# Optimization experiments

Measured on AMD Instinct MI355X. Metric: run time of the kernel, lower is better.

## Reference

```python
import jax, jax.numpy as jnp
import numpy as np

TABLE_SIZE = 524288
NUM_LEVELS = 16
MIN_RES = 16
MAX_RES = 2048
FEAT = 2
N_POINTS = 1048576

# Spatial-hash primes, wrapped to int32 exactly as the original module ends up doing
PRIMES = jnp.asarray(np.array([1, 2654435761, 805459861], dtype=np.uint32).astype(np.int32))

# Per-level grid resolutions (computed in float64 numpy at trace time, stored f32)
_levels_np = np.arange(NUM_LEVELS)
_growth = np.exp((np.log(MAX_RES) - np.log(MIN_RES)) / (NUM_LEVELS - 1))
SCALINGS = jnp.asarray(np.floor(MIN_RES * _growth ** _levels_np), dtype=jnp.float32)  # (L,)
HASH_OFFSET = jnp.arange(NUM_LEVELS, dtype=jnp.int32) * TABLE_SIZE  # (L,)

# Ceil(1)/floor(0) selector per corner, matching vertex_0..vertex_7 in the original
SEL = jnp.asarray(np.array([
    [1, 1, 1], [1, 1, 0], [1, 0, 1], [0, 1, 1],
    [1, 0, 0], [0, 1, 0], [0, 0, 1], [0, 0, 0]], dtype=bool))  # (8,3)


def setup_inputs() -> dict:
    key = jax.random.key(0)
    k1, k2 = jax.random.split(key)
    x = jax.random.uniform(k1, (N_POINTS, 3), dtype=jnp.float32)  # points in [0,1)^3
    hash_table = jax.random.normal(k2, (FEAT, TABLE_SIZE * NUM_LEVELS), dtype=jnp.float32)
    return {"x": x, "hash_table": hash_table}


def reference(x, hash_table):
    N = x.shape[0]
    scaled = x[:, None, :] * SCALINGS[None, :, None]          # (N, L, 3)
    c = jnp.ceil(scaled).astype(jnp.int32)                    # (N, L, 3)
    f = jnp.floor(scaled).astype(jnp.int32)                   # (N, L, 3)
    # Faithful to original: reshape (L,3)->(3,L), not a transpose
    po = (scaled - f).reshape(N, 3, NUM_LEVELS)               # (N, 3, L)

    # All 8 corner vertices at once: (N, 8, L, 3)
    verts = jnp.where(SEL[None, :, None, :], c[:, None], f[:, None])

    # Spatial hash with int32 wraparound, xor-fold over the 3 coords
    pre = verts * PRIMES                                      # (N, 8, L, 3) int32
    h = pre[..., 0] ^ pre[..., 1] ^ pre[..., 2]
    h = h % TABLE_SIZE + HASH_OFFSET                          # (N, 8, L), nonneg mod

    # Irregular gather from the table: (N, 8, L, F)
    feats = hash_table.T[h]

    px = po[:, 0, :, None]  # (N, L, 1)
    py = po[:, 1, :, None]
    pz = po[:, 2, :, None]

    f03 = feats[:, 0] * px + feats[:, 3] * (1 - px)
    f12 = feats[:, 1] * px + feats[:, 2] * (1 - px)
    f56 = feats[:, 5] * px + feats[:, 6] * (1 - px)
    f47 = feats[:, 4] * px + feats[:, 7] * (1 - px)
    f0312 = f03 * py + f12 * (1 - py)
    f4756 = f47 * py + f56 * (1 - py)
    enc = f0312 * pz + f4756 * (1 - pz)                       # (N, L, F)

    # Original returns ravel(transpose((F,L))) == (L,F) flattened, level-major
    return enc.reshape(N, NUM_LEVELS * FEAT)
```

## Files before the change

### kernel.cpp

```cpp
#include <hip/hip_runtime.h>
#include <hip/hip_fp16.h>

#define TS 524288u
#define NENT (TS * 16u)
#define FSTR NENT
#define NPTS 1048576u
#define P1 2654435761u
#define P2 805459861u
#define DMAXL 5

__device__ const float SCAL[16] = {
    16.f, 22.f, 30.f, 42.f, 58.f, 80.f, 111.f, 153.f,
    212.f, 294.f, 406.f, 561.f, 776.f, 1072.f, 1482.f, 2048.f
};
__device__ const unsigned CCUM[6] = {4096u, 14744u, 41744u, 115832u, 310944u, 822944u};
__device__ const unsigned VCUM[6] = {4913u, 17080u, 46871u, 126378u, 331757u, 863198u};
__device__ const unsigned DBASE[6] = {0u, 32768u, 117952u, 333952u, 926656u, 2487552u};
__device__ const unsigned VBASE[6] = {0u, 4913u, 17080u, 46871u, 126378u, 331757u};

#define NCELLS 822944u
#define NVERTS 863198u
#define DNB    26334208u
#define DVB    3452792u

__device__ inline unsigned bfp(float f) {
    unsigned u = __float_as_uint(f);
    return (u + 0x7FFFu + ((u >> 16) & 1u)) >> 16;
}
__device__ inline float blo(unsigned g) { return __uint_as_float(g << 16); }
__device__ inline float bhi(unsigned g) { return __uint_as_float(g & 0xFFFF0000u); }

__global__ __launch_bounds__(256) void pack_kernel(
    const float* __restrict__ tab, unsigned* __restrict__ tp)
{
    const unsigned i = (blockIdx.x * 256u + threadIdx.x) * 4u;
    const float4 a = *reinterpret_cast<const float4*>(tab + i);
    const float4 b = *reinterpret_cast<const float4*>(tab + i + FSTR);
    uint4 r;
    r.x = bfp(a.x) | (bfp(b.x) << 16);
    r.y = bfp(a.y) | (bfp(b.y) << 16);
    r.z = bfp(a.z) | (bfp(b.z) << 16);
    r.w = bfp(a.w) | (bfp(b.w) << 16);
    *reinterpret_cast<uint4*>(tp + i) = r;
}

__global__ __launch_bounds__(256) void vbuild_kernel(
    const unsigned* __restrict__ tp, unsigned* __restrict__ dv)
{
    const unsigned t = blockIdx.x * 256u + threadIdx.x;
    if (t >= NVERTS) return;
    unsigned lv = 0, base = 0;
#pragma unroll
    for (int l = 0; l < DMAXL; ++l)
        if (t >= VCUM[l]) { lv = l + 1; base = VCUM[l]; }
    const unsigned vid = t - base;
    const unsigned Rp = (unsigned)SCAL[lv] + 1u;
    const unsigned i = vid % Rp;
    const unsigned r1 = vid / Rp;
    const unsigned j = r1 % Rp;
    const unsigned k = r1 / Rp;
    const unsigned h = ((i ^ (j * P1) ^ (k * P2)) & (TS - 1u)) + lv * TS;
    dv[VBASE[lv] + vid] = tp[h];
}

__global__ __launch_bounds__(256) void cbuild_kernel(
    const unsigned* __restrict__ dv, unsigned* __restrict__ dn)
{
    const unsigned t = blockIdx.x * 256u + threadIdx.x;
    if (t >= NCELLS) return;
    unsigned lv = 0, base = 0;
#pragma unroll
    for (int l = 0; l < DMAXL; ++l)
        if (t >= CCUM[l]) { lv = l + 1; base = CCUM[l]; }
    const unsigned cid = t - base;
    const unsigned R = (unsigned)SCAL[lv];
    const unsigned Rp = R + 1u;
    const unsigned B0 = cid % R;
    const unsigned r1 = cid / R;
    const unsigned B1 = r1 % R;
    const unsigned B2 = r1 / R;
    const unsigned* v = dv + VBASE[lv];
    const unsigned vb = (B2 * Rp + B1) * Rp + B0;
    const unsigned sy = Rp, sz = Rp * Rp;
    const unsigned w0 = v[vb + 1u + sy + sz];
    const unsigned w1 = v[vb + 1u + sy];
    const unsigned w2 = v[vb + 1u + sz];
    const unsigned w3 = v[vb + sy + sz];
    const unsigned w4 = v[vb + 1u];
    const unsigned w5 = v[vb + sy];
    const unsigned w6 = v[vb + sz];
    const unsigned w7 = v[vb];
    uint4* dst = reinterpret_cast<uint4*>(dn + DBASE[lv] + cid * 8u);
    dst[0] = make_uint4(w0, w1, w2, w3);
    dst[1] = make_uint4(w4, w5, w6, w7);
}

template <int DENSE>
__global__ __launch_bounds__(256) void gather_kernel(
    const float* __restrict__ x,
    const unsigned* __restrict__ tp,
    const unsigned* __restrict__ dn,
    __half2* __restrict__ dst)
{
    const unsigned lv = blockIdx.x >> 12;
    const unsigned n  = (blockIdx.x & 4095u) * 256u + threadIdx.x;

    const float x0 = x[3u * n + 0u];
    const float x1 = x[3u * n + 1u];
    const float x2 = x[3u * n + 2u];

    const float S = SCAL[lv];
    const float s0 = x0 * S, s1 = x1 * S, s2 = x2 * S;
    const unsigned m = TS - 1u;
    const unsigned tbase = lv * TS;

    unsigned g0, g1, g2, g3, g4, g5, g6, g7;

    if ((int)lv <= DENSE) {
        const float f0 = floorf(s0), f1 = floorf(s1), f2 = floorf(s2);
        const unsigned B0 = (unsigned)(int)f0;
        const unsigned B1 = (unsigned)(int)f1;
        const unsigned B2 = (unsigned)(int)f2;
        const unsigned R = (unsigned)S;
        const unsigned cid = (B2 * R + B1) * R + B0;
        const uint4* blk = reinterpret_cast<const uint4*>(dn + DBASE[lv] + cid * 8u);
        const uint4 lo = blk[0];
        const uint4 hi = blk[1];
        g0 = lo.x; g1 = lo.y; g2 = lo.z; g3 = lo.w;
        g4 = hi.x; g5 = hi.y; g6 = hi.z; g7 = hi.w;
        const bool ex = (s0 == f0) | (s1 == f1) | (s2 == f2);
        if (__builtin_expect(__any(ex), 0)) {
            if (ex) {
                const unsigned A0 = (unsigned)(int)ceilf(s0);
                const unsigned a1 = (unsigned)(int)ceilf(s1) * P1, b1 = B1 * P1;
                const unsigned a2 = (unsigned)(int)ceilf(s2) * P2, b2 = B2 * P2;
                g0 = tp[((A0 ^ a1 ^ a2) & m) + tbase];
                g1 = tp[((A0 ^ a1 ^ b2) & m) + tbase];
                g2 = tp[((A0 ^ b1 ^ a2) & m) + tbase];
                g3 = tp[((B0 ^ a1 ^ a2) & m) + tbase];
                g4 = tp[((A0 ^ b1 ^ b2) & m) + tbase];
                g5 = tp[((B0 ^ a1 ^ b2) & m) + tbase];
                g6 = tp[((B0 ^ b1 ^ a2) & m) + tbase];
                g7 = tp[((B0 ^ b1 ^ b2) & m) + tbase];
            }
        }
    } else {
        const unsigned A0 = (unsigned)(int)ceilf(s0);
        const unsigned B0 = (unsigned)(int)floorf(s0);
        const unsigned a1 = (unsigned)(int)ceilf(s1) * P1;
        const unsigned b1 = (unsigned)(int)floorf(s1) * P1;
        const unsigned a2 = (unsigned)(int)ceilf(s2) * P2;
        const unsigned b2 = (unsigned)(int)floorf(s2) * P2;
        g0 = tp[((A0 ^ a1 ^ a2) & m) + tbase];
        g1 = tp[((A0 ^ a1 ^ b2) & m) + tbase];
        g2 = tp[((A0 ^ b1 ^ a2) & m) + tbase];
        g3 = tp[((B0 ^ a1 ^ a2) & m) + tbase];
        g4 = tp[((A0 ^ b1 ^ b2) & m) + tbase];
        g5 = tp[((B0 ^ a1 ^ b2) & m) + tbase];
        g6 = tp[((B0 ^ b1 ^ a2) & m) + tbase];
        g7 = tp[((B0 ^ b1 ^ b2) & m) + tbase];
    }

    float w[3];
#pragma unroll
    for (int i = 0; i < 3; ++i) {
        const unsigned k = lv + 16u * i;
        const unsigned lev = k / 3u, dim = k % 3u;
        const float xv = (dim == 0u) ? x0 : ((dim == 1u) ? x1 : x2);
        const float t = xv * SCAL[lev];
        w[i] = t - floorf(t);
    }
    const float wa = w[0], wb = w[1], wc = w[2];
    const float qa = 1.f - wa, qb = 1.f - wb, qc = 1.f - wc;

    const float e0 = ((blo(g0) * wa + blo(g3) * qa) * wb + (blo(g1) * wa + blo(g2) * qa) * qb) * wc
                   + ((blo(g4) * wa + blo(g7) * qa) * wb + (blo(g5) * wa + blo(g6) * qa) * qb) * qc;
    const float e1 = ((bhi(g0) * wa + bhi(g3) * qa) * wb + (bhi(g1) * wa + bhi(g2) * qa) * qb) * wc
                   + ((bhi(g4) * wa + bhi(g7) * qa) * wb + (bhi(g5) * wa + bhi(g6) * qa) * qb) * qc;

    dst[lv * NPTS + n] = __floats2half2_rn(e0, e1);
}

__global__ __launch_bounds__(256) void transpose_kernel(
    const __half2* __restrict__ enc, float4* __restrict__ out)
{
    const unsigned n = blockIdx.x * 256u + threadIdx.x;
    float2 v[16];
#pragma unroll
    for (int lv = 0; lv < 16; ++lv) v[lv] = __half22float2(enc[lv * NPTS + n]);
#pragma unroll
    for (int k = 0; k < 8; ++k)
        out[n * 8u + k] = make_float4(v[2 * k].x, v[2 * k].y, v[2 * k + 1].x, v[2 * k + 1].y);
}

__global__ __launch_bounds__(256) void hashenc_fallback(
    const float* __restrict__ x,
    const float* __restrict__ tab,
    float2* __restrict__ out)
{
    const unsigned tid = blockIdx.x * 256u + threadIdx.x;
    const unsigned n = tid >> 4;
    const unsigned l = tid & 15u;
    const float x0 = x[3u * n], x1 = x[3u * n + 1u], x2 = x[3u * n + 2u];
    const float S = SCAL[l];
    const float s0 = x0 * S, s1 = x1 * S, s2 = x2 * S;
    const unsigned A0 = (unsigned)(int)ceilf(s0);
    const unsigned B0 = (unsigned)(int)floorf(s0);
    const unsigned a1 = (unsigned)(int)ceilf(s1) * P1;
    const unsigned b1 = (unsigned)(int)floorf(s1) * P1;
    const unsigned a2 = (unsigned)(int)ceilf(s2) * P2;
    const unsigned b2 = (unsigned)(int)floorf(s2) * P2;
    const unsigned m = TS - 1u;
    const unsigned base = l * TS;
    const unsigned i0 = ((A0 ^ a1 ^ a2) & m) + base;
    const unsigned i1 = ((A0 ^ a1 ^ b2) & m) + base;
    const unsigned i2 = ((A0 ^ b1 ^ a2) & m) + base;
    const unsigned i3 = ((B0 ^ a1 ^ a2) & m) + base;
    const unsigned i4 = ((A0 ^ b1 ^ b2) & m) + base;
    const unsigned i5 = ((B0 ^ a1 ^ b2) & m) + base;
    const unsigned i6 = ((B0 ^ b1 ^ a2) & m) + base;
    const unsigned i7 = ((B0 ^ b1 ^ b2) & m) + base;
    const float a0v = tab[i0], a1v = tab[i1], a2v = tab[i2], a3v = tab[i3];
    const float a4v = tab[i4], a5v = tab[i5], a6v = tab[i6], a7v = tab[i7];
    const float b0v = tab[i0 + FSTR], b1v = tab[i1 + FSTR], b2v = tab[i2 + FSTR], b3v = tab[i3 + FSTR];
    const float b4v = tab[i4 + FSTR], b5v = tab[i5 + FSTR], b6v = tab[i6 + FSTR], b7v = tab[i7 + FSTR];
    float w[3];
#pragma unroll
    for (int i = 0; i < 3; ++i) {
        const unsigned k = l + 16u * i;
        const unsigned lev = k / 3u, dim = k % 3u;
        const float xv = (dim == 0u) ? x0 : ((dim == 1u) ? x1 : x2);
        const float t = xv * SCAL[lev];
        w[i] = t - floorf(t);
    }
    const float wa = w[0], wb = w[1], wc = w[2];
    const float qa = 1.f - wa, qb = 1.f - wb, qc = 1.f - wc;
    const float e0 = ((a0v * wa + a3v * qa) * wb + (a1v * wa + a2v * qa) * qb) * wc
                   + ((a4v * wa + a7v * qa) * wb + (a5v * wa + a6v * qa) * qb) * qc;
    const float e1 = ((b0v * wa + b3v * qa) * wb + (b1v * wa + b2v * qa) * qb) * wc
                   + ((b4v * wa + b7v * qa) * wb + (b5v * wa + b6v * qa) * qb) * qc;
    out[tid] = make_float2(e0, e1);
}

extern "C" void kernel_launch(void* const* d_in, const int* in_sizes, int n_in,
                              void* d_out, int out_size, void* d_ws, size_t ws_size,
                              hipStream_t stream) {
    const float* x   = (const float*)d_in[0];
    const float* tab = (const float*)d_in[1];
    char* ws = (char*)d_ws;

    const size_t packB = (size_t)NENT * 4u;
    const size_t scrB  = (size_t)NPTS * 16u * 4u;
    const size_t need_dense = packB + (size_t)DNB + (size_t)DVB + scrB;
    const size_t need_plain = packB + scrB;

    if (ws_size >= need_dense) {
        unsigned* tp = (unsigned*)ws;
        unsigned* dn = (unsigned*)(ws + packB);
        unsigned* dv = (unsigned*)(ws + packB + DNB);
        __half2*  sc = (__half2*)(ws + packB + DNB + DVB);
        pack_kernel<<<NENT / 4u / 256u, 256, 0, stream>>>(tab, tp);
        vbuild_kernel<<<(NVERTS + 255u) / 256u, 256, 0, stream>>>(tp, dv);
        cbuild_kernel<<<(NCELLS + 255u) / 256u, 256, 0, stream>>>(dv, dn);
        gather_kernel<DMAXL><<<16 * 4096, 256, 0, stream>>>(x, tp, dn, sc);
        transpose_kernel<<<NPTS / 256u, 256, 0, stream>>>(sc, (float4*)d_out);
    } else if (ws_size >= need_plain) {
        unsigned* tp = (unsigned*)ws;
        __half2*  sc = (__half2*)(ws + packB);
        pack_kernel<<<NENT / 4u / 256u, 256, 0, stream>>>(tab, tp);
        gather_kernel<-1><<<16 * 4096, 256, 0, stream>>>(x, tp, tp, sc);
        transpose_kernel<<<NPTS / 256u, 256, 0, stream>>>(sc, (float4*)d_out);
    } else {
        hashenc_fallback<<<NPTS * 16u / 256u, 256, 0, stream>>>(x, tab, (float2*)d_out);
    }
}
```

Measured before the change: 528.1 us.

## Fuse per-level gather and transpose into one per-point kernel over all levels

Replaces the level-major gather kernel plus separate transpose kernel with a single kernel in which each thread handles a point (two points per thread via a loop), computing all 16 levels and writing the final float row directly with nontemporal vector stores. This removes the fp16 scratch buffer write and re-read and one kernel launch. The trade-off is lost locality: previously all threads in a launch wave touched the same level's table, while now each thread hits 16 different levels' tables, which may hurt cache hit rates for the random gathers. Register pressure and occupancy also change, and each thread now issues more outstanding loads.

```diff
diff --git a/kernel.cpp b/kernel.cpp
--- a/kernel.cpp
+++ b/kernel.cpp
@@ -5,9 +5,12 @@
 #define NENT (TS * 16u)
 #define FSTR NENT
 #define NPTS 1048576u
+#define NTHREADS 524288u
 #define P1 2654435761u
 #define P2 805459861u
 #define DMAXL 5
+
+typedef float f32x4 __attribute__((ext_vector_type(4)));
 
 __device__ const float SCAL[16] = {
     16.f, 22.f, 30.f, 42.f, 58.f, 80.f, 111.f, 153.f,
@@ -96,44 +99,64 @@
 }
 
 template <int DENSE>
-__global__ __launch_bounds__(256) void gather_kernel(
+__global__ __launch_bounds__(256) void fused_kernel(
     const float* __restrict__ x,
     const unsigned* __restrict__ tp,
     const unsigned* __restrict__ dn,
-    __half2* __restrict__ dst)
-{
-    const unsigned lv = blockIdx.x >> 12;
-    const unsigned n  = (blockIdx.x & 4095u) * 256u + threadIdx.x;
-
-    const float x0 = x[3u * n + 0u];
-    const float x1 = x[3u * n + 1u];
-    const float x2 = x[3u * n + 2u];
-
-    const float S = SCAL[lv];
-    const float s0 = x0 * S, s1 = x1 * S, s2 = x2 * S;
-    const unsigned m = TS - 1u;
-    const unsigned tbase = lv * TS;
-
-    unsigned g0, g1, g2, g3, g4, g5, g6, g7;
-
-    if ((int)lv <= DENSE) {
-        const float f0 = floorf(s0), f1 = floorf(s1), f2 = floorf(s2);
-        const unsigned B0 = (unsigned)(int)f0;
-        const unsigned B1 = (unsigned)(int)f1;
-        const unsigned B2 = (unsigned)(int)f2;
-        const unsigned R = (unsigned)S;
-        const unsigned cid = (B2 * R + B1) * R + B0;
-        const uint4* blk = reinterpret_cast<const uint4*>(dn + DBASE[lv] + cid * 8u);
-        const uint4 lo = blk[0];
-        const uint4 hi = blk[1];
-        g0 = lo.x; g1 = lo.y; g2 = lo.z; g3 = lo.w;
-        g4 = hi.x; g5 = hi.y; g6 = hi.z; g7 = hi.w;
-        const bool ex = (s0 == f0) | (s1 == f1) | (s2 == f2);
-        if (__builtin_expect(__any(ex), 0)) {
-            if (ex) {
+    float* __restrict__ out)
+{
+    const unsigned t0 = blockIdx.x * 256u + threadIdx.x;
+#pragma unroll 1
+    for (unsigned c = 0; c < NPTS / NTHREADS; ++c) {
+        const unsigned n = t0 + c * NTHREADS;
+        const float x0 = x[3u * n + 0u];
+        const float x1 = x[3u * n + 1u];
+        const float x2 = x[3u * n + 2u];
+
+        __half2 enc[16];
+#pragma unroll
+        for (int lv = 0; lv < 16; ++lv) {
+            const float S = SCAL[lv];
+            const float s0 = x0 * S, s1 = x1 * S, s2 = x2 * S;
+            const unsigned m = TS - 1u;
+            const unsigned tbase = (unsigned)lv * TS;
+
+            unsigned g0, g1, g2, g3, g4, g5, g6, g7;
+            if (lv <= DENSE) {
+                const float f0 = floorf(s0), f1 = floorf(s1), f2 = floorf(s2);
+                const unsigned B0 = (unsigned)(int)f0;
+                const unsigned B1 = (unsigned)(int)f1;
+                const unsigned B2 = (unsigned)(int)f2;
+                const unsigned R = (unsigned)S;
+                const unsigned cid = (B2 * R + B1) * R + B0;
+                const uint4* blk = reinterpret_cast<const uint4*>(dn + DBASE[lv] + cid * 8u);
+                const uint4 lo = blk[0];
+                const uint4 hi = blk[1];
+                g0 = lo.x; g1 = lo.y; g2 = lo.z; g3 = lo.w;
+                g4 = hi.x; g5 = hi.y; g6 = hi.z; g7 = hi.w;
+                const bool ex = (s0 == f0) | (s1 == f1) | (s2 == f2);
+                if (__builtin_expect(__any(ex), 0)) {
+                    if (ex) {
+                        const unsigned A0 = (unsigned)(int)ceilf(s0);
+                        const unsigned a1 = (unsigned)(int)ceilf(s1) * P1, b1 = B1 * P1;
+                        const unsigned a2 = (unsigned)(int)ceilf(s2) * P2, b2 = B2 * P2;
+                        g0 = tp[((A0 ^ a1 ^ a2) & m) + tbase];
+                        g1 = tp[((A0 ^ a1 ^ b2) & m) + tbase];
+                        g2 = tp[((A0 ^ b1 ^ a2) & m) + tbase];
+                        g3 = tp[((B0 ^ a1 ^ a2) & m) + tbase];
+                        g4 = tp[((A0 ^ b1 ^ b2) & m) + tbase];
+                        g5 = tp[((B0 ^ a1 ^ b2) & m) + tbase];
+                        g6 = tp[((B0 ^ b1 ^ a2) & m) + tbase];
+                        g7 = tp[((B0 ^ b1 ^ b2) & m) + tbase];
+                    }
+                }
+            } else {
                 const unsigned A0 = (unsigned)(int)ceilf(s0);
-                const unsigned a1 = (unsigned)(int)ceilf(s1) * P1, b1 = B1 * P1;
-                const unsigned a2 = (unsigned)(int)ceilf(s2) * P2, b2 = B2 * P2;
+                const unsigned B0 = (unsigned)(int)floorf(s0);
+                const unsigned a1 = (unsigned)(int)ceilf(s1) * P1;
+                const unsigned b1 = (unsigned)(int)floorf(s1) * P1;
+                const unsigned a2 = (unsigned)(int)ceilf(s2) * P2;
+                const unsigned b2 = (unsigned)(int)floorf(s2) * P2;
                 g0 = tp[((A0 ^ a1 ^ a2) & m) + tbase];
                 g1 = tp[((A0 ^ a1 ^ b2) & m) + tbase];
                 g2 = tp[((A0 ^ b1 ^ a2) & m) + tbase];
@@ -143,54 +166,35 @@
                 g6 = tp[((B0 ^ b1 ^ a2) & m) + tbase];
                 g7 = tp[((B0 ^ b1 ^ b2) & m) + tbase];
             }
+
+            float w[3];
+#pragma unroll
+            for (int i = 0; i < 3; ++i) {
+                const int k = lv + 16 * i;
+                const int lev = k / 3, dim = k % 3;
+                const float xv = (dim == 0) ? x0 : ((dim == 1) ? x1 : x2);
+                const float t = xv * SCAL[lev];
+                w[i] = t - floorf(t);
+            }
+            const float wa = w[0], wb = w[1], wc = w[2];
+            const float qa = 1.f - wa, qb = 1.f - wb, qc = 1.f - wc;
+
+            const float e0 = ((blo(g0) * wa + blo(g3) * qa) * wb + (blo(g1) * wa + blo(g2) * qa) * qb) * wc
+                           + ((blo(g4) * wa + blo(g7) * qa) * wb + (blo(g5) * wa + blo(g6) * qa) * qb) * qc;
+            const float e1 = ((bhi(g0) * wa + bhi(g3) * qa) * wb + (bhi(g1) * wa + bhi(g2) * qa) * qb) * wc
+                           + ((bhi(g4) * wa + bhi(g7) * qa) * wb + (bhi(g5) * wa + bhi(g6) * qa) * qb) * qc;
+            enc[lv] = __floats2half2_rn(e0, e1);
         }
-    } else {
-        const unsigned A0 = (unsigned)(int)ceilf(s0);
-        const unsigned B0 = (unsigned)(int)floorf(s0);
-        const unsigned a1 = (unsigned)(int)ceilf(s1) * P1;
-        const unsigned b1 = (unsigned)(int)floorf(s1) * P1;
-        const unsigned a2 = (unsigned)(int)ceilf(s2) * P2;
-        const unsigned b2 = (unsigned)(int)floorf(s2) * P2;
-        g0 = tp[((A0 ^ a1 ^ a2) & m) + tbase];
-        g1 = tp[((A0 ^ a1 ^ b2) & m) + tbase];
-        g2 = tp[((A0 ^ b1 ^ a2) & m) + tbase];
-        g3 = tp[((B0 ^ a1 ^ a2) & m) + tbase];
-        g4 = tp[((A0 ^ b1 ^ b2) & m) + tbase];
-        g5 = tp[((B0 ^ a1 ^ b2) & m) + tbase];
-        g6 = tp[((B0 ^ b1 ^ a2) & m) + tbase];
-        g7 = tp[((B0 ^ b1 ^ b2) & m) + tbase];
+
+        f32x4* o = reinterpret_cast<f32x4*>(out + (size_t)n * 32u);
+#pragma unroll
+        for (int k = 0; k < 8; ++k) {
+            const float2 a = __half22float2(enc[2 * k]);
+            const float2 b = __half22float2(enc[2 * k + 1]);
+            f32x4 v = {a.x, a.y, b.x, b.y};
+            __builtin_nontemporal_store(v, o + k);
+        }
     }
-
-    float w[3];
-#pragma unroll
-    for (int i = 0; i < 3; ++i) {
-        const unsigned k = lv + 16u * i;
-        const unsigned lev = k / 3u, dim = k % 3u;
-        const float xv = (dim == 0u) ? x0 : ((dim == 1u) ? x1 : x2);
-        const float t = xv * SCAL[lev];
-        w[i] = t - floorf(t);
-    }
-    const float wa = w[0], wb = w[1], wc = w[2];
-    const float qa = 1.f - wa, qb = 1.f - wb, qc = 1.f - wc;
-
-    const float e0 = ((blo(g0) * wa + blo(g3) * qa) * wb + (blo(g1) * wa + blo(g2) * qa) * qb) * wc
-                   + ((blo(g4) * wa + blo(g7) * qa) * wb + (blo(g5) * wa + blo(g6) * qa) * qb) * qc;
-    const float e1 = ((bhi(g0) * wa + bhi(g3) * qa) * wb + (bhi(g1) * wa + bhi(g2) * qa) * qb) * wc
-                   + ((bhi(g4) * wa + bhi(g7) * qa) * wb + (bhi(g5) * wa + bhi(g6) * qa) * qb) * qc;
-
-    dst[lv * NPTS + n] = __floats2half2_rn(e0, e1);
-}
-
-__global__ __launch_bounds__(256) void transpose_kernel(
-    const __half2* __restrict__ enc, float4* __restrict__ out)
-{
-    const unsigned n = blockIdx.x * 256u + threadIdx.x;
-    float2 v[16];
-#pragma unroll
-    for (int lv = 0; lv < 16; ++lv) v[lv] = __half22float2(enc[lv * NPTS + n]);
-#pragma unroll
-    for (int k = 0; k < 8; ++k)
-        out[n * 8u + k] = make_float4(v[2 * k].x, v[2 * k].y, v[2 * k + 1].x, v[2 * k + 1].y);
 }
 
 __global__ __launch_bounds__(256) void hashenc_fallback(
@@ -250,26 +254,21 @@
     char* ws = (char*)d_ws;
 
     const size_t packB = (size_t)NENT * 4u;
-    const size_t scrB  = (size_t)NPTS * 16u * 4u;
-    const size_t need_dense = packB + (size_t)DNB + (size_t)DVB + scrB;
-    const size_t need_plain = packB + scrB;
+    const size_t need_dense = packB + (size_t)DNB + (size_t)DVB;
+    const size_t need_plain = packB;
 
     if (ws_size >= need_dense) {
         unsigned* tp = (unsigned*)ws;
         unsigned* dn = (unsigned*)(ws + packB);
         unsigned* dv = (unsigned*)(ws + packB + DNB);
-        __half2*  sc = (__half2*)(ws + packB + DNB + DVB);
         pack_kernel<<<NENT / 4u / 256u, 256, 0, stream>>>(tab, tp);
         vbuild_kernel<<<(NVERTS + 255u) / 256u, 256, 0, stream>>>(tp, dv);
         cbuild_kernel<<<(NCELLS + 255u) / 256u, 256, 0, stream>>>(dv, dn);
-        gather_kernel<DMAXL><<<16 * 4096, 256, 0, stream>>>(x, tp, dn, sc);
-        transpose_kernel<<<NPTS / 256u, 256, 0, stream>>>(sc, (float4*)d_out);
+        fused_kernel<DMAXL><<<NTHREADS / 256u, 256, 0, stream>>>(x, tp, dn, (float*)d_out);
     } else if (ws_size >= need_plain) {
         unsigned* tp = (unsigned*)ws;
-        __half2*  sc = (__half2*)(ws + packB);
         pack_kernel<<<NENT / 4u / 256u, 256, 0, stream>>>(tab, tp);
-        gather_kernel<-1><<<16 * 4096, 256, 0, stream>>>(x, tp, tp, sc);
-        transpose_kernel<<<NPTS / 256u, 256, 0, stream>>>(sc, (float4*)d_out);
+        fused_kernel<-1><<<NTHREADS / 256u, 256, 0, stream>>>(x, tp, tp, (float*)d_out);
     } else {
         hashenc_fallback<<<NPTS * 16u / 256u, 256, 0, stream>>>(x, tab, (float2*)d_out);
     }
```

Result: slower. 787.0 us (+49.0%).
